# Performance work log

Measured on AMD Instinct MI355X. Metric: run time of the kernel, lower is better.

Reference implementation:

```python
import jax, jax.numpy as jnp
import numpy as np
import math

FACTOR = 5

def setup_inputs() -> dict:
    key = jax.random.key(0)
    kq, kk, kv = jax.random.split(key, 3)
    B, L, H, D = 2, 4096, 8, 64
    queries = jax.random.normal(kq, (B, L, H, D), dtype=jnp.float32)
    keys = jax.random.normal(kk, (B, L, H, D), dtype=jnp.float32)
    values = jax.random.normal(kv, (B, L, H, D), dtype=jnp.float32)
    attn_mask = jnp.ones((B, L), dtype=jnp.int32)
    return {"queries": queries, "keys": keys, "values": values, "attn_mask": attn_mask}

def reference(queries, keys, values, attn_mask):
    B, L_Q, H, D = queries.shape
    L_K = keys.shape[1]
    # [B, L, H, D] -> [B, H, L, D]
    Q = jnp.transpose(queries, (0, 2, 1, 3))
    K = jnp.transpose(keys, (0, 2, 1, 3))
    V = jnp.transpose(values, (0, 2, 1, 3))

    U_part = max(min(FACTOR * int(math.ceil(math.log(max(L_K, 1)))), L_K), 1)
    u = max(min(FACTOR * int(math.ceil(math.log(max(L_Q, 1)))), L_Q), 1)

    # random key sampling per query (torch.randint replaced by fixed jax key)
    idx = jax.random.randint(jax.random.key(1), (L_Q, U_part), 0, L_K)  # [L_Q, S]
    K_sample = K[:, :, idx, :]  # [B, H, L_Q, S, D]  (irregular gather)
    Q_K_sample = jnp.einsum('bhqd,bhqsd->bhqs', Q, K_sample)  # [B, H, L_Q, S]

    # sparsity measure M = max - mean(full-length normalization L_K as in source)
    M = Q_K_sample.max(axis=-1) - Q_K_sample.sum(axis=-1) / L_K  # [B, H, L_Q]
    _, M_top = jax.lax.top_k(M, u)  # [B, H, u]

    Q_reduce = jnp.take_along_axis(Q, M_top[..., None], axis=2)  # [B, H, u, D]
    scale = 1.0 / math.sqrt(D)
    scores = jnp.einsum('bhud,bhkd->bhuk', Q_reduce, K) * scale  # [B, H, u, L_K]

    mask = attn_mask[:, None, None, :]  # [B,1,1,L_K]
    scores = jnp.where(mask == 0, -jnp.inf, scores)

    A = jax.nn.softmax(scores, axis=-1)  # dropout p=0 -> identity
    context = jnp.einsum('bhuk,bhkd->bhud', A, V)  # [B, H, u, D]
    return jnp.transpose(context, (0, 2, 1, 3))  # [B, u, H, D]
```

## Files before the change

kernel.cpp:

```cpp
#include <hip/hip_runtime.h>
#include <math.h>

#define JAX_PARTITIONABLE 1

constexpr int Bc = 2, Lc = 4096, Hc = 8, Dc = 64;
constexpr int BHc = Bc * Hc;
constexpr int Uc = 45;
constexpr int NSc = 45;

typedef float vfloat4 __attribute__((ext_vector_type(4)));

struct TF2 { unsigned a, b; };

__host__ __device__ constexpr unsigned rotl32(unsigned v, int n) {
  return (v << n) | (v >> (32 - n));
}

__host__ __device__ constexpr TF2 tf2(unsigned k0, unsigned k1, unsigned x0, unsigned x1) {
  unsigned ks2 = k0 ^ k1 ^ 0x1BD11BDAu;
  x0 += k0; x1 += k1;
  x0 += x1; x1 = rotl32(x1, 13); x1 ^= x0;
  x0 += x1; x1 = rotl32(x1, 15); x1 ^= x0;
  x0 += x1; x1 = rotl32(x1, 26); x1 ^= x0;
  x0 += x1; x1 = rotl32(x1, 6);  x1 ^= x0;
  x0 += k1; x1 += ks2 + 1u;
  x0 += x1; x1 = rotl32(x1, 17); x1 ^= x0;
  x0 += x1; x1 = rotl32(x1, 29); x1 ^= x0;
  x0 += x1; x1 = rotl32(x1, 16); x1 ^= x0;
  x0 += x1; x1 = rotl32(x1, 24); x1 ^= x0;
  x0 += ks2; x1 += k0 + 2u;
  x0 += x1; x1 = rotl32(x1, 13); x1 ^= x0;
  x0 += x1; x1 = rotl32(x1, 15); x1 ^= x0;
  x0 += x1; x1 = rotl32(x1, 26); x1 ^= x0;
  x0 += x1; x1 = rotl32(x1, 6);  x1 ^= x0;
  x0 += k0; x1 += k1 + 3u;
  x0 += x1; x1 = rotl32(x1, 17); x1 ^= x0;
  x0 += x1; x1 = rotl32(x1, 29); x1 ^= x0;
  x0 += x1; x1 = rotl32(x1, 16); x1 ^= x0;
  x0 += x1; x1 = rotl32(x1, 24); x1 ^= x0;
  x0 += k1; x1 += ks2 + 4u;
  x0 += x1; x1 = rotl32(x1, 13); x1 ^= x0;
  x0 += x1; x1 = rotl32(x1, 15); x1 ^= x0;
  x0 += x1; x1 = rotl32(x1, 26); x1 ^= x0;
  x0 += x1; x1 = rotl32(x1, 6);  x1 ^= x0;
  x0 += ks2; x1 += k0 + 5u;
  return TF2{x0, x1};
}

template <int CTRL>
__device__ __forceinline__ float dpp_add(float x) {
  int t = __builtin_amdgcn_update_dpp(0, __float_as_int(x), CTRL, 0xF, 0xF, false);
  return x + __int_as_float(t);
}
template <int CTRL>
__device__ __forceinline__ float dpp_idf(float x) {
  int t = __builtin_amdgcn_update_dpp(__float_as_int(x), __float_as_int(x), CTRL, 0xF, 0xF, false);
  return __int_as_float(t);
}
__device__ __forceinline__ float wave_max_bcast(float x) {
  x = fmaxf(x, dpp_idf<0x111>(x));
  x = fmaxf(x, dpp_idf<0x112>(x));
  x = fmaxf(x, dpp_idf<0x114>(x));
  x = fmaxf(x, dpp_idf<0x118>(x));
  x = fmaxf(x, dpp_idf<0x142>(x));
  x = fmaxf(x, dpp_idf<0x143>(x));
  return __int_as_float(__builtin_amdgcn_readlane(__float_as_int(x), 63));
}
__device__ __forceinline__ float wave_sum_bcast(float x) {
  x = dpp_add<0x111>(x);
  x = dpp_add<0x112>(x);
  x = dpp_add<0x114>(x);
  x = dpp_add<0x118>(x);
  x = dpp_add<0x142>(x);
  x = dpp_add<0x143>(x);
  return __int_as_float(__builtin_amdgcn_readlane(__float_as_int(x), 63));
}

__device__ __forceinline__ float dot4_acc(float4 q, float4 k, float a) {
  a = fmaf(q.x, k.x, a);
  a = fmaf(q.y, k.y, a);
  a = fmaf(q.z, k.z, a);
  a = fmaf(q.w, k.w, a);
  return a;
}

__global__ __launch_bounds__(256) void k_scoreM(const float* __restrict__ Q, const float* __restrict__ K,
                                                float* __restrict__ M) {
  __shared__ int sidx[720];
  int tid = threadIdx.x;
  int bx = blockIdx.x;
  int bh = bx & 15;
  int qblk = bx >> 4;
  int b = bh >> 3, h = bh & 7;
  int lane16 = tid & 15, qloc = tid >> 4;
  int q = qblk * 16 + qloc;
  constexpr TF2 kb = tf2(0u, 1u, 0u, 1u);
  for (int e = tid; e < 720; e += 256) {
    TF2 r = tf2(kb.a, kb.b, 0u, (unsigned)(qblk * 720 + e));
    sidx[e] = (int)((r.a ^ r.b) & 4095u);
  }
  __syncthreads();
  const vfloat4* Q4 = (const vfloat4*)Q;
  const vfloat4* K4 = (const vfloat4*)K;
  vfloat4 qr = Q4[((b * Lc + q) * Hc + h) * 16 + lane16];
  int kbase = (b * Lc * Hc + h) * 16 + lane16;
  const int* ip = sidx + qloc * NSc;
  float mx = -INFINITY, sm = 0.f;
  #pragma unroll
  for (int s0 = 0; s0 < NSc; s0 += 5) {
    int kk[5];
    #pragma unroll
    for (int i = 0; i < 5; ++i) kk[i] = ip[s0 + i];
    vfloat4 kv[5];
    #pragma unroll
    for (int i = 0; i < 5; ++i) kv[i] = __builtin_nontemporal_load(&K4[kbase + kk[i] * (Hc * 16)]);
    #pragma unroll
    for (int i = 0; i < 5; ++i) {
      float p = fmaf(qr[0], kv[i][0], fmaf(qr[1], kv[i][1], fmaf(qr[2], kv[i][2], qr[3] * kv[i][3])));
      p = dpp_add<0x111>(p);
      p = dpp_add<0x112>(p);
      p = dpp_add<0x114>(p);
      p = dpp_add<0x118>(p);
      mx = fmaxf(mx, p);
      sm += p;
    }
  }
  if (lane16 == 15) M[bh * Lc + q] = mx - sm * (1.0f / Lc);
}

__global__ __launch_bounds__(256) void k_topk(const float* __restrict__ M, const float* __restrict__ Q,
                                              int* __restrict__ topk, float* __restrict__ qg) {
  __shared__ unsigned su[Lc];
  __shared__ int hist[256];
  __shared__ int sfx[257];
  __shared__ unsigned s_prefix;
  __shared__ int s_r;
  __shared__ int n_gt, n_eq;
  __shared__ unsigned cu[64];
  __shared__ int cidx[64];
  __shared__ int eqi[64];
  __shared__ int srank[Uc];
  int bh = blockIdx.x, tid = threadIdx.x;
  int b = bh >> 3, h = bh & 7;
  const float* m = M + bh * Lc;
  for (int e = tid; e < Lc; e += 256) {
    unsigned bb = __float_as_uint(m[e]);
    su[e] = (bb & 0x80000000u) ? ~bb : (bb | 0x80000000u);
  }
  if (tid == 0) { s_r = Uc; s_prefix = 0u; n_gt = 0; n_eq = 0; }
  __syncthreads();
  #pragma unroll
  for (int p = 0; p < 4; ++p) {
    int shift = 24 - 8 * p;
    hist[tid] = 0;
    __syncthreads();
    unsigned pref = s_prefix;
    unsigned hmask = (p == 0) ? 0u : (0xFFFFFFFFu << (shift + 8));
    for (int e = tid; e < Lc; e += 256) {
      unsigned u = su[e];
      if ((u & hmask) == pref) atomicAdd(&hist[(u >> shift) & 255u], 1);
    }
    __syncthreads();
    sfx[tid] = hist[tid];
    __syncthreads();
    for (int off = 1; off < 256; off <<= 1) {
      int v = (tid + off < 256) ? sfx[tid + off] : 0;
      __syncthreads();
      sfx[tid] += v;
      __syncthreads();
    }
    int r = s_r;
    __syncthreads();
    int above = (tid < 255) ? sfx[tid + 1] : 0;
    if (sfx[tid] >= r && above < r) {
      s_r = r - above;
      s_prefix = pref | ((unsigned)tid << shift);
    }
    __syncthreads();
  }
  unsigned T = s_prefix;
  int rf = s_r;
  for (int e = tid; e < Lc; e += 256) {
    unsigned u = su[e];
    if (u > T) {
      int p = atomicAdd(&n_gt, 1);
      cu[p] = u; cidx[p] = e;
    } else if (u == T) {
      int p = atomicAdd(&n_eq, 1);
      if (p < 64) eqi[p] = e;
    }
  }
  __syncthreads();
  int ne = n_eq < 64 ? n_eq : 64;
  if (tid < ne) {
    int myi = eqi[tid];
    int rank = 0;
    for (int j = 0; j < ne; ++j) rank += (eqi[j] < myi);
    if (rank < rf) {
      int p = atomicAdd(&n_gt, 1);
      cu[p] = T; cidx[p] = myi;
    }
  }
  __syncthreads();
  if (tid < Uc) {
    unsigned mu = cu[tid]; int mi = cidx[tid];
    int rank = 0;
    for (int j = 0; j < Uc; ++j) {
      unsigned ju = cu[j]; int ji = cidx[j];
      rank += (ju > mu) || (ju == mu && ji < mi);
    }
    topk[bh * Uc + rank] = mi;
    srank[rank] = mi;
  }
  __syncthreads();
  const float4* Q4 = (const float4*)Q;
  float4* qg4 = (float4*)qg;
  for (int e = tid; e < Uc * 16; e += 256) {
    int t = e >> 4, dq = e & 15;
    qg4[bh * Uc * 16 + e] = Q4[((b * Lc + srank[t]) * Hc + h) * 16 + dq];
  }
}

template<int NC>
__global__ __launch_bounds__(256) void k_attn(const float* __restrict__ qg, const float* __restrict__ K,
                                              const float* __restrict__ V, const int* __restrict__ amask,
                                              float* __restrict__ pO, float* __restrict__ pM,
                                              float* __restrict__ pL) {
  constexpr int CH = Lc / NC;
  constexpr int TG = 256 / CH;
  constexpr int SCW = CH + 4;
  int chunk = blockIdx.x, bh = blockIdx.y;
  int b = bh >> 3, h = bh & 7;
  int tid = threadIdx.x;
  __shared__ __align__(16) float qs[Uc * 64];
  __shared__ __align__(16) float sc[48][SCW];
  {
    const float4* qg4 = (const float4*)qg;
    float4* qs4w = (float4*)qs;
    for (int e = tid; e < Uc * 16; e += 256) qs4w[e] = qg4[bh * Uc * 16 + e];
  }
  for (int e = tid; e < 3 * SCW; e += 256) sc[45 + e / SCW][e % SCW] = 0.f;
  __syncthreads();
  {
    int k = tid % CH, tg = tid / CH;
    int key = chunk * CH + k;
    const float4* K4 = (const float4*)K;
    int kb = ((b * Lc + key) * Hc + h) * 16;
    float4 kr[16];
    #pragma unroll
    for (int j = 0; j < 16; ++j) kr[j] = K4[kb + j];
    int mk = amask[b * Lc + key];
    const float4* qs4 = (const float4*)qs;
    for (int t = tg; t < Uc; t += TG) {
      float a0 = 0.f, a1 = 0.f, a2 = 0.f, a3 = 0.f;
      #pragma unroll
      for (int j = 0; j < 16; j += 4) {
        a0 = dot4_acc(qs4[t * 16 + j],     kr[j],     a0);
        a1 = dot4_acc(qs4[t * 16 + j + 1], kr[j + 1], a1);
        a2 = dot4_acc(qs4[t * 16 + j + 2], kr[j + 2], a2);
        a3 = dot4_acc(qs4[t * 16 + j + 3], kr[j + 3], a3);
      }
      float acc = (a0 + a1) + (a2 + a3);
      sc[t][k] = mk ? acc * 0.125f : -INFINITY;
    }
  }
  __syncthreads();
  {
    int w = tid >> 6, lane = tid & 63;
    for (int t = w; t < Uc; t += 4) {
      float x = sc[t][lane];
      float ml = wave_max_bcast(x);
      float p = (ml != -INFINITY) ? __expf(x - ml) : 0.f;
      sc[t][lane] = p;
      float ls = wave_sum_bcast(p);
      if (lane == 0) {
        pM[(bh * NC + chunk) * Uc + t] = ml;
        pL[(bh * NC + chunk) * Uc + t] = ls;
      }
    }
  }
  __syncthreads();
  {
    int ty = tid >> 4, tx = tid & 15;
    float4 o0 = {0.f, 0.f, 0.f, 0.f};
    float4 o1 = {0.f, 0.f, 0.f, 0.f};
    float4 o2 = {0.f, 0.f, 0.f, 0.f};
    const float4* V4 = (const float4*)V;
    const float4* s0 = (const float4*)&sc[ty][0];
    const float4* s1 = (const float4*)&sc[ty + 16][0];
    const float4* s2 = (const float4*)&sc[ty + 32][0];
    int vbase = (b * Lc + chunk * CH) * (Hc * 16) + h * 16 + tx;
    #pragma unroll 2
    for (int kq = 0; kq < CH / 4; ++kq) {
      float4 p0 = s0[kq], p1 = s1[kq], p2 = s2[kq];
      float4 va = V4[vbase + (4 * kq + 0) * (Hc * 16)];
      float4 vb = V4[vbase + (4 * kq + 1) * (Hc * 16)];
      float4 vc = V4[vbase + (4 * kq + 2) * (Hc * 16)];
      float4 vd = V4[vbase + (4 * kq + 3) * (Hc * 16)];
      o0.x = fmaf(p0.x, va.x, o0.x); o0.y = fmaf(p0.x, va.y, o0.y); o0.z = fmaf(p0.x, va.z, o0.z); o0.w = fmaf(p0.x, va.w, o0.w);
      o1.x = fmaf(p1.x, va.x, o1.x); o1.y = fmaf(p1.x, va.y, o1.y); o1.z = fmaf(p1.x, va.z, o1.z); o1.w = fmaf(p1.x, va.w, o1.w);
      o2.x = fmaf(p2.x, va.x, o2.x); o2.y = fmaf(p2.x, va.y, o2.y); o2.z = fmaf(p2.x, va.z, o2.z); o2.w = fmaf(p2.x, va.w, o2.w);
      o0.x = fmaf(p0.y, vb.x, o0.x); o0.y = fmaf(p0.y, vb.y, o0.y); o0.z = fmaf(p0.y, vb.z, o0.z); o0.w = fmaf(p0.y, vb.w, o0.w);
      o1.x = fmaf(p1.y, vb.x, o1.x); o1.y = fmaf(p1.y, vb.y, o1.y); o1.z = fmaf(p1.y, vb.z, o1.z); o1.w = fmaf(p1.y, vb.w, o1.w);
      o2.x = fmaf(p2.y, vb.x, o2.x); o2.y = fmaf(p2.y, vb.y, o2.y); o2.z = fmaf(p2.y, vb.z, o2.z); o2.w = fmaf(p2.y, vb.w, o2.w);
      o0.x = fmaf(p0.z, vc.x, o0.x); o0.y = fmaf(p0.z, vc.y, o0.y); o0.z = fmaf(p0.z, vc.z, o0.z); o0.w = fmaf(p0.z, vc.w, o0.w);
      o1.x = fmaf(p1.z, vc.x, o1.x); o1.y = fmaf(p1.z, vc.y, o1.y); o1.z = fmaf(p1.z, vc.z, o1.z); o1.w = fmaf(p1.z, vc.w, o1.w);
      o2.x = fmaf(p2.z, vc.x, o2.x); o2.y = fmaf(p2.z, vc.y, o2.y); o2.z = fmaf(p2.z, vc.z, o2.z); o2.w = fmaf(p2.z, vc.w, o2.w);
      o0.x = fmaf(p0.w, vd.x, o0.x); o0.y = fmaf(p0.w, vd.y, o0.y); o0.z = fmaf(p0.w, vd.z, o0.z); o0.w = fmaf(p0.w, vd.w, o0.w);
      o1.x = fmaf(p1.w, vd.x, o1.x); o1.y = fmaf(p1.w, vd.y, o1.y); o1.z = fmaf(p1.w, vd.z, o1.z); o1.w = fmaf(p1.w, vd.w, o1.w);
      o2.x = fmaf(p2.w, vd.x, o2.x); o2.y = fmaf(p2.w, vd.y, o2.y); o2.z = fmaf(p2.w, vd.z, o2.z); o2.w = fmaf(p2.w, vd.w, o2.w);
    }
    float4* pO4 = (float4*)pO;
    int obase = ((bh * NC + chunk) * Uc) * 16 + tx;
    pO4[obase + ty * 16] = o0;
    pO4[obase + (ty + 16) * 16] = o1;
    if (ty < 13) pO4[obase + (ty + 32) * 16] = o2;
  }
}

template<int NC>
__global__ __launch_bounds__(256) void k_merge(const float* __restrict__ pO, const float* __restrict__ pM,
                                               const float* __restrict__ pL, float* __restrict__ out) {
  int f = blockIdx.x * 256 + threadIdx.x;
  int d = f & 63, h = (f >> 6) & 7;
  int bt = f >> 9;
  int t = bt % Uc, b = bt / Uc;
  int bh = b * 8 + h;
  float m = -INFINITY;
  for (int c = 0; c < NC; ++c) m = fmaxf(m, pM[(bh * NC + c) * Uc + t]);
  float den = 0.f, num = 0.f;
  for (int c = 0; c < NC; ++c) {
    float mc = pM[(bh * NC + c) * Uc + t];
    float wgt = (mc == -INFINITY) ? 0.f : __expf(mc - m);
    den += wgt * pL[(bh * NC + c) * Uc + t];
    num += wgt * pO[((bh * NC + c) * Uc + t) * 64 + d];
  }
  out[f] = num / den;
}

extern "C" void kernel_launch(void* const* d_in, const int* in_sizes, int n_in,
                              void* d_out, int out_size, void* d_ws, size_t ws_size,
                              hipStream_t stream) {
  const float* Q = (const float*)d_in[0];
  const float* K = (const float*)d_in[1];
  const float* V = (const float*)d_in[2];
  const int* amask = (const int*)d_in[3];
  float* out = (float*)d_out;
  char* ws = (char*)d_ws;
  float* M    = (float*)(ws + 0x000000);
  int*   topk = (int*)(ws + 0x040000);
  float* qg   = (float*)(ws + 0x041000);
  float* pM   = (float*)(ws + 0x070000);
  size_t need64 = 0x70000UL + 64UL * 190080UL;
  size_t need32 = 0x70000UL + 32UL * 190080UL;
  int NC = ws_size >= need64 ? 64 : (ws_size >= need32 ? 32 : 16);
  float* pL = pM + 16 * NC * Uc;
  float* pO = pL + 16 * NC * Uc;

  k_scoreM<<<4096, 256, 0, stream>>>(Q, K, M);
  k_topk<<<BHc, 256, 0, stream>>>(M, Q, topk, qg);
  if (NC == 64) {
    k_attn<64><<<dim3(64, BHc), 256, 0, stream>>>(qg, K, V, amask, pO, pM, pL);
    k_merge<64><<<180, 256, 0, stream>>>(pO, pM, pL, out);
  } else if (NC == 32) {
    k_attn<32><<<dim3(32, BHc), 256, 0, stream>>>(qg, K, V, amask, pO, pM, pL);
    k_merge<32><<<180, 256, 0, stream>>>(pO, pM, pL, out);
  } else {
    k_attn<16><<<dim3(16, BHc), 256, 0, stream>>>(qg, K, V, amask, pO, pM, pL);
    k_merge<16><<<180, 256, 0, stream>>>(pO, pM, pL, out);
  }
}
```

Measured before the change: 178.8 us.

## Bucket sampled key indices by chunk and compute sampled scores from LDS

The sampled-score step no longer gathers random K rows per query. Four kernels now do the work: one generates the sample indices, one buckets them per query into 32 key chunks, one stages each K chunk in LDS and computes partial max/sum for every query against its bucketed samples, and one merges the partials into M. The aim is to turn scattered global K reads into coalesced chunk loads with reuse from LDS. In exchange it adds three launches, a large partial buffer plus index table in workspace, and serial per-query loops. Samples beyond 12 per chunk are silently dropped.

Result: slower. 341.1 us (+90.8%).

```diff
diff --git a/kernel.cpp b/kernel.cpp
--- a/kernel.cpp
+++ b/kernel.cpp
@@ -7,6 +7,9 @@
 constexpr int BHc = Bc * Hc;
 constexpr int Uc = 45;
 constexpr int NSc = 45;
+constexpr int NKC = 32;
+constexpr int KROWS = Lc / NKC;
+constexpr int BCAP = 12;
 
 typedef float vfloat4 __attribute__((ext_vector_type(4)));
 
@@ -84,48 +87,87 @@
   return a;
 }
 
-__global__ __launch_bounds__(256) void k_scoreM(const float* __restrict__ Q, const float* __restrict__ K,
-                                                float* __restrict__ M) {
-  __shared__ int sidx[720];
+__global__ __launch_bounds__(256) void k_idx(int* __restrict__ idx) {
+  int f = blockIdx.x * 256 + threadIdx.x;
+  constexpr TF2 kb = tf2(0u, 1u, 0u, 1u);
+  TF2 r = tf2(kb.a, kb.b, 0u, (unsigned)f);
+  idx[f] = (int)((r.a ^ r.b) & 4095u);
+}
+
+__global__ __launch_bounds__(128) void k_bucket(const int* __restrict__ idx, uint4* __restrict__ gtable) {
+  __shared__ unsigned char loc[128][NKC][BCAP];
+  __shared__ unsigned char cnt[128][NKC];
   int tid = threadIdx.x;
-  int bx = blockIdx.x;
-  int bh = bx & 15;
-  int qblk = bx >> 4;
+  int q = blockIdx.x * 128 + tid;
+  for (int c = 0; c < NKC; ++c) cnt[tid][c] = 0;
+  const int* ip = idx + q * NSc;
+  for (int s = 0; s < NSc; ++s) {
+    int k = ip[s];
+    int c = k >> 7;
+    int n = cnt[tid][c];
+    if (n < BCAP) { loc[tid][c][n] = (unsigned char)(k & 127); cnt[tid][c] = (unsigned char)(n + 1); }
+  }
+  for (int c = 0; c < NKC; ++c) {
+    int n = cnt[tid][c];
+    unsigned w0 = 0, w1 = 0, w2 = 0;
+    for (int j = 0; j < BCAP; ++j) {
+      unsigned v = (j < n) ? (unsigned)loc[tid][c][j] : 0u;
+      if (j < 4) w0 |= v << (8 * j);
+      else if (j < 8) w1 |= v << (8 * (j - 4));
+      else w2 |= v << (8 * (j - 8));
+    }
+    gtable[c * Lc + q] = make_uint4(w0, w1, w2, (unsigned)n);
+  }
+}
+
+__global__ __launch_bounds__(256) void k_scoreMb(const float* __restrict__ Q, const float* __restrict__ K,
+                                                 const uint4* __restrict__ gtable, float2* __restrict__ part) {
+  __shared__ __align__(16) float ldsK[KROWS * 64];
+  int bh = blockIdx.x, c = blockIdx.y;
   int b = bh >> 3, h = bh & 7;
-  int lane16 = tid & 15, qloc = tid >> 4;
-  int q = qblk * 16 + qloc;
-  constexpr TF2 kb = tf2(0u, 1u, 0u, 1u);
-  for (int e = tid; e < 720; e += 256) {
-    TF2 r = tf2(kb.a, kb.b, 0u, (unsigned)(qblk * 720 + e));
-    sidx[e] = (int)((r.a ^ r.b) & 4095u);
-  }
-  __syncthreads();
-  const vfloat4* Q4 = (const vfloat4*)Q;
-  const vfloat4* K4 = (const vfloat4*)K;
-  vfloat4 qr = Q4[((b * Lc + q) * Hc + h) * 16 + lane16];
-  int kbase = (b * Lc * Hc + h) * 16 + lane16;
-  const int* ip = sidx + qloc * NSc;
+  int tid = threadIdx.x, lane16 = tid & 15, gid = tid >> 4;
+  const float4* K4 = (const float4*)K;
+  float4* lk4 = (float4*)ldsK;
+  for (int r = gid; r < KROWS; r += 16)
+    lk4[r * 16 + lane16] = K4[((b * Lc + c * KROWS + r) * Hc + h) * 16 + lane16];
+  __syncthreads();
+  const float4* Q4 = (const float4*)Q;
+  const float4* lkr = (const float4*)ldsK;
+  int qbase = gid * 256;
+  for (int qo = 0; qo < 256; ++qo) {
+    int q = qbase + qo;
+    uint4 t = gtable[c * Lc + q];
+    int n = (int)t.w;
+    float mx = -INFINITY, sm = 0.f;
+    if (n) {
+      float4 qr = Q4[((b * Lc + q) * Hc + h) * 16 + lane16];
+      for (int j = 0; j < n; ++j) {
+        unsigned wv = (j < 4) ? t.x : (j < 8) ? t.y : t.z;
+        int k8 = (int)((wv >> ((j & 3) * 8)) & 255u);
+        float4 kv = lkr[k8 * 16 + lane16];
+        float p = fmaf(qr.x, kv.x, fmaf(qr.y, kv.y, fmaf(qr.z, kv.z, qr.w * kv.w)));
+        p = dpp_add<0x111>(p);
+        p = dpp_add<0x112>(p);
+        p = dpp_add<0x114>(p);
+        p = dpp_add<0x118>(p);
+        mx = fmaxf(mx, p);
+        sm += p;
+      }
+    }
+    if (lane16 == 15) part[(bh * NKC + c) * Lc + q] = make_float2(mx, sm);
+  }
+}
+
+__global__ __launch_bounds__(256) void k_scoreMerge(const float2* __restrict__ part, float* __restrict__ M) {
+  int g = blockIdx.x * 256 + threadIdx.x;
+  int q = g & (Lc - 1), bh = g >> 12;
   float mx = -INFINITY, sm = 0.f;
-  #pragma unroll
-  for (int s0 = 0; s0 < NSc; s0 += 5) {
-    int kk[5];
-    #pragma unroll
-    for (int i = 0; i < 5; ++i) kk[i] = ip[s0 + i];
-    vfloat4 kv[5];
-    #pragma unroll
-    for (int i = 0; i < 5; ++i) kv[i] = __builtin_nontemporal_load(&K4[kbase + kk[i] * (Hc * 16)]);
-    #pragma unroll
-    for (int i = 0; i < 5; ++i) {
-      float p = fmaf(qr[0], kv[i][0], fmaf(qr[1], kv[i][1], fmaf(qr[2], kv[i][2], qr[3] * kv[i][3])));
-      p = dpp_add<0x111>(p);
-      p = dpp_add<0x112>(p);
-      p = dpp_add<0x114>(p);
-      p = dpp_add<0x118>(p);
-      mx = fmaxf(mx, p);
-      sm += p;
-    }
-  }
-  if (lane16 == 15) M[bh * Lc + q] = mx - sm * (1.0f / Lc);
+  for (int c = 0; c < NKC; ++c) {
+    float2 p = part[(bh * NKC + c) * Lc + q];
+    mx = fmaxf(mx, p.x);
+    sm += p.y;
+  }
+  M[bh * Lc + q] = mx - sm * (1.0f / Lc);
 }
 
 __global__ __launch_bounds__(256) void k_topk(const float* __restrict__ M, const float* __restrict__ Q,
@@ -347,17 +389,23 @@
   const int* amask = (const int*)d_in[3];
   float* out = (float*)d_out;
   char* ws = (char*)d_ws;
-  float* M    = (float*)(ws + 0x000000);
-  int*   topk = (int*)(ws + 0x040000);
-  float* qg   = (float*)(ws + 0x041000);
-  float* pM   = (float*)(ws + 0x070000);
-  size_t need64 = 0x70000UL + 64UL * 190080UL;
-  size_t need32 = 0x70000UL + 32UL * 190080UL;
+  int*    idx    = (int*)(ws + 0x0000000);
+  uint4*  gtable = (uint4*)(ws + 0x00B4000);
+  float2* part   = (float2*)(ws + 0x02B4000);
+  float*  M      = (float*)(ws + 0x12B4000);
+  int*    topk   = (int*)(ws + 0x12F4000);
+  float*  qg     = (float*)(ws + 0x12F5000);
+  float*  pM     = (float*)(ws + 0x1330000);
+  size_t need64 = 0x1330000UL + 64UL * 190080UL;
+  size_t need32 = 0x1330000UL + 32UL * 190080UL;
   int NC = ws_size >= need64 ? 64 : (ws_size >= need32 ? 32 : 16);
   float* pL = pM + 16 * NC * Uc;
   float* pO = pL + 16 * NC * Uc;
 
-  k_scoreM<<<4096, 256, 0, stream>>>(Q, K, M);
+  k_idx<<<720, 256, 0, stream>>>(idx);
+  k_bucket<<<32, 128, 0, stream>>>(idx, gtable);
+  k_scoreMb<<<dim3(BHc, NKC), 256, 0, stream>>>(Q, K, gtable, part);
+  k_scoreMerge<<<256, 256, 0, stream>>>(part, M);
   k_topk<<<BHc, 256, 0, stream>>>(M, Q, topk, qg);
   if (NC == 64) {
     k_attn<64><<<dim3(64, BHc), 256, 0, stream>>>(qg, K, V, amask, pO, pM, pL);
```
